# Kernel optimization log

Measured on AMD Instinct MI355X. Metric: run time of the kernel, lower is better.

The kernel has to match this reference:

```python
import jax, jax.numpy as jnp
import numpy as np

N_NODES = 100000
N_EDGES = 3200000
N_GRAPHS = 128
F_IN, HID = 16, 64


def setup_inputs() -> dict:
    key = jax.random.key(0)
    ks = jax.random.split(key, 16)
    def lin(k, fan_in, fan_out):
        bound = 1.0 / np.sqrt(fan_in)
        kw, kb = jax.random.split(k)
        W = jax.random.uniform(kw, (fan_in, fan_out), jnp.float32, -bound, bound)
        b = jax.random.uniform(kb, (fan_out,), jnp.float32, -bound, bound)
        return W, b
    x = jax.random.normal(ks[0], (N_NODES, F_IN), jnp.float32)
    edge_index = jax.random.randint(ks[1], (2, N_EDGES), 0, N_NODES, jnp.int64 if jax.config.jax_enable_x64 else jnp.int32)
    edge_attr = jax.random.normal(ks[2], (N_EDGES, 4), jnp.float32)
    batch = jnp.sort(jax.random.randint(ks[3], (N_NODES,), 0, N_GRAPHS))
    W1, b1 = lin(ks[4], F_IN, HID)
    W2, b2 = lin(ks[5], HID, HID)
    W3, b3 = lin(ks[6], HID, HID)
    Wf1, bf1 = lin(ks[7], HID, 32)
    Wf2, bf2 = lin(ks[8], 32, 1)
    return dict(x=x, edge_index=edge_index, edge_attr=edge_attr, batch=batch,
                W1=W1, b1=b1, W2=W2, b2=b2, W3=W3, b3=b3,
                Wf1=Wf1, bf1=bf1, Wf2=Wf2, bf2=bf2)


def _gcn_conv(x, src, dst, norm, W, b, n_nodes):
    # PyG GCNConv: out = scatter_add(norm * (x @ W)[src] -> dst) + b
    h = x @ W                                   # [N, out]
    msg = h[src] * norm[:, None]                # [E+N, out] gather + scale
    agg = jax.ops.segment_sum(msg, dst, num_segments=n_nodes)
    return agg + b


def reference(x, edge_index, edge_attr, batch, W1, b1, W2, b2, W3, b3, Wf1, bf1, Wf2, bf2):
    n = x.shape[0]
    # add self loops (GCNConv default)
    loop = jnp.arange(n, dtype=edge_index.dtype)
    src = jnp.concatenate([edge_index[0], loop])
    dst = jnp.concatenate([edge_index[1], loop])
    # symmetric degree normalization: deg computed on dst with self loops
    deg = jax.ops.segment_sum(jnp.ones_like(src, dtype=x.dtype), dst, num_segments=n)
    dinv = jax.lax.rsqrt(jnp.maximum(deg, 1.0))
    norm = dinv[src] * dinv[dst]

    h = jax.nn.relu(_gcn_conv(x, src, dst, norm, W1, b1, n))   # dropout = identity (eval)
    h = jax.nn.relu(_gcn_conv(h, src, dst, norm, W2, b2, n))
    h = jax.nn.relu(_gcn_conv(h, src, dst, norm, W3, b3, n))

    # global mean pool over graphs
    sums = jax.ops.segment_sum(h, batch, num_segments=N_GRAPHS)          # [B, HID]
    cnts = jax.ops.segment_sum(jnp.ones((n,), x.dtype), batch, num_segments=N_GRAPHS)
    pooled = sums / jnp.maximum(cnts, 1.0)[:, None]

    z = jax.nn.relu(pooled @ Wf1 + bf1)
    return z @ Wf2 + bf2                                                  # [B, 1]
```

## Files before the change

### kernel.cpp

```cpp
#include <hip/hip_runtime.h>
#include <hip/hip_bf16.h>

#define HID 64
#define MAXNB 2048
#define NBLK 512
#define FILL_T 1024
#define HREP 4

__device__ __forceinline__ float bf2f(unsigned short u) {
    return __uint_as_float(((unsigned)u) << 16);
}
__device__ __forceinline__ unsigned short f2bf(float f) {
    __hip_bfloat16 b = __float2bfloat16(f);
    return *(unsigned short*)&b;
}
__device__ __forceinline__ unsigned packbf(float lo, float hi) {
    return (unsigned)f2bf(lo) | ((unsigned)f2bf(hi) << 16);
}


__global__ __launch_bounds__(FILL_T) void radix_hist_kernel(
    const int* __restrict__ ei, int* __restrict__ H, int* __restrict__ bhist,
    int E, int NB, int C) {
    __shared__ int lh[HREP * (MAXNB + 1)];
    int blk = blockIdx.x, tid = threadIdx.x;
    for (int i = tid; i < HREP * (MAXNB + 1); i += FILL_T) lh[i] = 0;
    __syncthreads();
    int* lhr = lh + ((tid >> 6) & (HREP - 1)) * (MAXNB + 1);
    int lo = blk * C, hi = min(lo + C, E);
    int cnt = hi - lo;
    int n4 = ((E & 3) == 0) ? (cnt >> 2) : 0;
    const int4* d4 = (const int4*)(ei + (long long)E + lo);
    for (int k = tid; k < n4; k += FILL_T) {
        int4 d = d4[k];
        atomicAdd(&lhr[d.x >> 6], 1);
        atomicAdd(&lhr[d.y >> 6], 1);
        atomicAdd(&lhr[d.z >> 6], 1);
        atomicAdd(&lhr[d.w >> 6], 1);
    }
    for (int e = lo + (n4 << 2) + tid; e < hi; e += FILL_T)
        atomicAdd(&lhr[ei[(long long)E + e] >> 6], 1);
    __syncthreads();
    for (int i = tid; i < NB; i += FILL_T) {
        int v = 0;
#pragma unroll
        for (int r = 0; r < HREP; r++) v += lh[r * (MAXNB + 1) + i];
        H[blk * NB + i] = v;
        if (v) atomicAdd(&bhist[i], v);
    }
}

__global__ __launch_bounds__(256) void scan_kernel(
    const int* __restrict__ bhist, int* __restrict__ pptr, int* __restrict__ gcur, int NB) {
    __shared__ int ssum[256];
    int tid = threadIdx.x;
    int C = (NB + 255) / 256;
    int lo = tid * C, hi = min(lo + C, NB);
    int s = 0;
    for (int i = lo; i < hi; i++) s += bhist[i];
    ssum[tid] = s;
    __syncthreads();
    for (int off = 1; off < 256; off <<= 1) {
        int v = (tid >= off) ? ssum[tid - off] : 0;
        __syncthreads();
        ssum[tid] += v;
        __syncthreads();
    }
    int run = (tid == 0) ? 0 : ssum[tid - 1];
    for (int i = lo; i < hi; i++) {
        pptr[i] = run;
        gcur[i] = run;
        run += bhist[i];
    }
    if (hi == NB) pptr[NB] = run;
}

__global__ __launch_bounds__(FILL_T) void radix_fill_kernel(
    const int* __restrict__ ei, const int* __restrict__ H, int* __restrict__ gcur,
    unsigned* __restrict__ ebuf, int E, int NB, int C) {
    __shared__ int lcur[MAXNB];
    int blk = blockIdx.x, tid = threadIdx.x;
    for (int i = tid; i < NB; i += FILL_T) {
        int c = H[blk * NB + i];
        lcur[i] = c ? atomicAdd(&gcur[i], c) : 0;
    }
    __syncthreads();
    int lo = blk * C, hi = min(lo + C, E);
    int cnt = hi - lo;
    int n4 = ((E & 3) == 0) ? (cnt >> 2) : 0;
    const int4* s4 = (const int4*)(ei + lo);
    const int4* d4 = (const int4*)(ei + (long long)E + lo);
    for (int k = tid; k < n4; k += FILL_T) {
        int4 s = s4[k];
        int4 d = d4[k];
        int p0 = atomicAdd(&lcur[d.x >> 6], 1);
        int p1 = atomicAdd(&lcur[d.y >> 6], 1);
        int p2 = atomicAdd(&lcur[d.z >> 6], 1);
        int p3 = atomicAdd(&lcur[d.w >> 6], 1);
        ebuf[p0] = ((unsigned)s.x << 6) | (unsigned)(d.x & 63);
        ebuf[p1] = ((unsigned)s.y << 6) | (unsigned)(d.y & 63);
        ebuf[p2] = ((unsigned)s.z << 6) | (unsigned)(d.z & 63);
        ebuf[p3] = ((unsigned)s.w << 6) | (unsigned)(d.w & 63);
    }
    for (int e = lo + (n4 << 2) + tid; e < hi; e += FILL_T) {
        int s = ei[e];
        int d = ei[(long long)E + e];
        int pos = atomicAdd(&lcur[d >> 6], 1);
        ebuf[pos] = ((unsigned)s << 6) | (unsigned)(d & 63);
    }
}

__global__ __launch_bounds__(256) void node_csr_kernel(
    const int* __restrict__ pptr, const unsigned* __restrict__ ebuf,
    int* __restrict__ row_ptr, int* __restrict__ col, float* __restrict__ dinv,
    int N, int NB) {
    __shared__ int lcnt[64];
    __shared__ int loff[64];
    __shared__ int lcur[64];
    int bkt = blockIdx.x, tid = threadIdx.x;
    int beg = pptr[bkt], end = pptr[bkt + 1];
    if (tid < 64) lcnt[tid] = 0;
    __syncthreads();
    for (int e = beg + tid; e < end; e += 256) atomicAdd(&lcnt[ebuf[e] & 63u], 1);
    __syncthreads();
    if (tid < 64) {
        int v = lcnt[tid];
        int p = v;
#pragma unroll
        for (int off = 1; off < 64; off <<= 1) {
            int t = __shfl_up(p, off);
            if (tid >= off) p += t;
        }
        int base = beg + p - v;
        loff[tid] = base;
        lcur[tid] = base;
        int node = (bkt << 6) + tid;
        if (node < N) {
            row_ptr[node] = base;
            dinv[node] = rsqrtf((float)(v + 1));
        }
    }
    if (tid == 0 && bkt == NB - 1) row_ptr[N] = pptr[NB];
    __syncthreads();
    for (int e = beg + tid; e < end; e += 256) {
        unsigned ev = ebuf[e];
        int pos = atomicAdd(&lcur[ev & 63u], 1);
        col[pos] = (int)(ev >> 6);
    }
}

__global__ __launch_bounds__(256) void xs_kernel(
    const float* __restrict__ x, const float* __restrict__ dinv,
    unsigned short* __restrict__ xs, int N) {
    int n = blockIdx.x * 256 + threadIdx.x;
    if (n >= N) return;
    float dv = dinv[n];
    const float4* xr = (const float4*)(x + (long long)n * 16);
    float4 a = xr[0], b = xr[1], c = xr[2], d = xr[3];
    uint4 w;
    w.x = packbf(dv * a.x, dv * a.y);
    w.y = packbf(dv * a.z, dv * a.w);
    w.z = packbf(dv * b.x, dv * b.y);
    w.w = packbf(dv * b.z, dv * b.w);
    uint4 v;
    v.x = packbf(dv * c.x, dv * c.y);
    v.y = packbf(dv * c.z, dv * c.w);
    v.z = packbf(dv * d.x, dv * d.y);
    v.w = packbf(dv * d.z, dv * d.w);
    uint4* out = (uint4*)(xs + ((long long)n << 4));
    out[0] = w;
    out[1] = v;
}

__device__ __forceinline__ void add4(float* acc, uint2 r) {
    acc[0] += __uint_as_float(r.x << 16);
    acc[1] += __uint_as_float(r.x & 0xffff0000u);
    acc[2] += __uint_as_float(r.y << 16);
    acc[3] += __uint_as_float(r.y & 0xffff0000u);
}

__global__ __launch_bounds__(256) void gather16_kernel(
    const int* __restrict__ row_ptr, const int* __restrict__ col,
    const unsigned short* __restrict__ xs, float* __restrict__ agg, int N) {
    int wv = __builtin_amdgcn_readfirstlane(threadIdx.x >> 6);
    int node = blockIdx.x * 4 + wv;
    int lane = threadIdx.x & 63;
    if (node >= N) return;
    int grp = lane >> 2;
    int c = lane & 3;
    int beg = row_ptr[node], end = row_ptr[node + 1];

    float acc[4] = {0.f, 0.f, 0.f, 0.f};
    if (grp == 0) {
        uint2 rs = *(const uint2*)(xs + ((long long)node << 4) + (c << 2));
        add4(acc, rs);
    }
    for (int base = beg; base < end; base += 32) {
        int e0 = base + grp;
        int e1 = e0 + 16;
        bool k0 = e0 < end, k1 = e1 < end;
        int c0 = k0 ? col[e0] : 0;
        int c1 = k1 ? col[e1] : 0;
        uint2 r0 = *(const uint2*)(xs + (((long long)c0) << 4) + (c << 2));
        uint2 r1 = *(const uint2*)(xs + (((long long)c1) << 4) + (c << 2));
        if (k0) add4(acc, r0);
        if (k1) add4(acc, r1);
    }
#pragma unroll
    for (int m = 4; m <= 32; m <<= 1) {
#pragma unroll
        for (int k = 0; k < 4; k++) acc[k] += __shfl_xor(acc[k], m);
    }
    if (lane < 4) {
        float4 w = make_float4(acc[0], acc[1], acc[2], acc[3]);
        *(float4*)(agg + ((long long)node << 4) + (lane << 2)) = w;
    }
}

__global__ void gemm_agg_kernel(const float* __restrict__ agg,
                                const float* __restrict__ W,
                                const float* __restrict__ dinv,
                                const float* __restrict__ bias,
                                unsigned short* __restrict__ g, int N) {
    __shared__ float sW[16 * HID];
    __shared__ float sIn[16 * 16];
    __shared__ float sB[HID];
    int tid = threadIdx.x;
    for (int idx = tid; idx < 16 * HID; idx += 256) sW[idx] = W[idx];
    if (tid < HID) sB[tid] = bias[tid];
    int base = blockIdx.x * 16;
    if (tid < 256) {
        int r = tid / 16, cc = tid % 16;
        int node = base + r;
        sIn[tid] = (node < N) ? agg[(long long)node * 16 + cc] : 0.f;
    }
    __syncthreads();
    int j = tid & 63;
    int si = tid >> 6;
#pragma unroll
    for (int u = 0; u < 4; u++) {
        int r = si * 4 + u;
        int node = base + r;
        if (node >= N) continue;
        float acc = 0.f;
#pragma unroll
        for (int k = 0; k < 16; k++) acc += sIn[r * 16 + k] * sW[k * HID + j];
        float v = dinv[node] * acc + sB[j];
        g[(long long)node * HID + j] = f2bf(v > 0.f ? v : 0.f);
    }
}

template <typename Tin, int K>
__global__ void gemm_g_kernel(const Tin* __restrict__ in,
                              const float* __restrict__ W,
                              const float* __restrict__ dinv,
                              unsigned short* __restrict__ g, int N) {
    __shared__ float sW[K * HID];
    __shared__ float sIn[16 * K];
    int tid = threadIdx.x;
    for (int idx = tid; idx < K * HID; idx += 256) sW[idx] = W[idx];
    int base = blockIdx.x * 16;
    for (int idx = tid; idx < 16 * K; idx += 256) {
        int r = idx / K, c = idx % K;
        int node = base + r;
        float v = 0.f;
        if (node < N) {
            Tin t = in[(long long)node * K + c];
            if constexpr (sizeof(Tin) == 2) v = bf2f((unsigned short)t);
            else v = (float)t;
        }
        sIn[idx] = v;
    }
    __syncthreads();
    int j = tid & 63;
    int si = tid >> 6;
#pragma unroll
    for (int u = 0; u < 4; u++) {
        int r = si * 4 + u;
        int node = base + r;
        if (node >= N) continue;
        float acc = 0.f;
#pragma unroll
        for (int k = 0; k < K; k++) acc += sIn[r * K + k] * sW[k * HID + j];
        g[(long long)node * HID + j] = f2bf(dinv[node] * acc);
    }
}

__device__ __forceinline__ void add8(float* acc, uint4 r) {
    acc[0] += __uint_as_float(r.x << 16);
    acc[1] += __uint_as_float(r.x & 0xffff0000u);
    acc[2] += __uint_as_float(r.y << 16);
    acc[3] += __uint_as_float(r.y & 0xffff0000u);
    acc[4] += __uint_as_float(r.z << 16);
    acc[5] += __uint_as_float(r.z & 0xffff0000u);
    acc[6] += __uint_as_float(r.w << 16);
    acc[7] += __uint_as_float(r.w & 0xffff0000u);
}

__global__ __launch_bounds__(256) void gather_kernel(
    const int* __restrict__ row_ptr, const int* __restrict__ col,
    const unsigned short* __restrict__ g, const float* __restrict__ dinv,
    const float* __restrict__ bias, unsigned short* __restrict__ h, int N) {
    int wv = __builtin_amdgcn_readfirstlane(threadIdx.x >> 6);
    int node = blockIdx.x * 4 + wv;
    int lane = threadIdx.x & 63;
    if (node >= N) return;
    int grp = lane >> 3;
    int c = lane & 7;
    int beg = row_ptr[node], end = row_ptr[node + 1];

    float acc[8] = {0.f, 0.f, 0.f, 0.f, 0.f, 0.f, 0.f, 0.f};
    if (grp == 0) {
        uint4 rs = *(const uint4*)(g + ((long long)node << 6) + (c << 3));
        add8(acc, rs);
    }

    for (int base = beg; base < end; base += 32) {
        int e0 = base + grp;
        int e1 = e0 + 8, e2 = e0 + 16, e3 = e0 + 24;
        bool k0 = e0 < end, k1 = e1 < end, k2 = e2 < end, k3 = e3 < end;
        int c0 = k0 ? col[e0] : 0;
        int c1 = k1 ? col[e1] : 0;
        int c2 = k2 ? col[e2] : 0;
        int c3 = k3 ? col[e3] : 0;
        uint4 r0 = *(const uint4*)(g + (((long long)c0) << 6) + (c << 3));
        uint4 r1 = *(const uint4*)(g + (((long long)c1) << 6) + (c << 3));
        uint4 r2 = *(const uint4*)(g + (((long long)c2) << 6) + (c << 3));
        uint4 r3 = *(const uint4*)(g + (((long long)c3) << 6) + (c << 3));
        if (k0) add8(acc, r0);
        if (k1) add8(acc, r1);
        if (k2) add8(acc, r2);
        if (k3) add8(acc, r3);
    }

#pragma unroll
    for (int m = 8; m <= 32; m <<= 1) {
#pragma unroll
        for (int k = 0; k < 8; k++) acc[k] += __shfl_xor(acc[k], m);
    }

    if (lane < 8) {
        float dv = dinv[node];
        float4 ba = *(const float4*)(bias + (lane << 3));
        float4 bb = *(const float4*)(bias + (lane << 3) + 4);
        float v0 = dv * acc[0] + ba.x;
        float v1 = dv * acc[1] + ba.y;
        float v2 = dv * acc[2] + ba.z;
        float v3 = dv * acc[3] + ba.w;
        float v4 = dv * acc[4] + bb.x;
        float v5 = dv * acc[5] + bb.y;
        float v6 = dv * acc[6] + bb.z;
        float v7 = dv * acc[7] + bb.w;
        v0 = v0 > 0.f ? v0 : 0.f;
        v1 = v1 > 0.f ? v1 : 0.f;
        v2 = v2 > 0.f ? v2 : 0.f;
        v3 = v3 > 0.f ? v3 : 0.f;
        v4 = v4 > 0.f ? v4 : 0.f;
        v5 = v5 > 0.f ? v5 : 0.f;
        v6 = v6 > 0.f ? v6 : 0.f;
        v7 = v7 > 0.f ? v7 : 0.f;
        uint4 w;
        w.x = (unsigned)f2bf(v0) | ((unsigned)f2bf(v1) << 16);
        w.y = (unsigned)f2bf(v2) | ((unsigned)f2bf(v3) << 16);
        w.z = (unsigned)f2bf(v4) | ((unsigned)f2bf(v5) << 16);
        w.w = (unsigned)f2bf(v6) | ((unsigned)f2bf(v7) << 16);
        *(uint4*)(h + ((long long)node << 6) + (lane << 3)) = w;
    }
}

__global__ void pool_kernel(const unsigned short* __restrict__ h, const int* __restrict__ batch,
                            float* __restrict__ sums, float* __restrict__ cnt, int N) {
    int wave = blockIdx.x * 4 + (threadIdx.x >> 6);
    int lane = threadIdx.x & 63;
    int lo = wave * 16;
    if (lo >= N) return;
    int hi = min(lo + 16, N);
    int curb = batch[lo];
    float sum = 0.f;
    int nseg = 0;
    for (int i = lo; i < hi; i++) {
        int b = batch[i];
        if (b != curb) {
            atomicAdd(&sums[curb * HID + lane], sum);
            if (lane == 0) atomicAdd(&cnt[curb], (float)nseg);
            curb = b; sum = 0.f; nseg = 0;
        }
        sum += bf2f(h[(long long)i * HID + lane]);
        nseg++;
    }
    atomicAdd(&sums[curb * HID + lane], sum);
    if (lane == 0) atomicAdd(&cnt[curb], (float)nseg);
}

__global__ void final_kernel(const float* __restrict__ sums, const float* __restrict__ cnt,
                             const float* __restrict__ Wf1, const float* __restrict__ bf1,
                             const float* __restrict__ Wf2, const float* __restrict__ bf2,
                             float* __restrict__ out) {
    __shared__ float sW1[HID * 32];
    __shared__ float sW2[32];
    int tid = threadIdx.x;
    for (int idx = tid; idx < HID * 32; idx += 128) sW1[idx] = Wf1[idx];
    if (tid < 32) sW2[tid] = Wf2[tid];
    __syncthreads();
    int b = tid;
    float pooled[HID];
    float c = fmaxf(cnt[b], 1.0f);
#pragma unroll
    for (int j = 0; j < HID; j++) pooled[j] = sums[b * HID + j] / c;
    float o = bf2[0];
#pragma unroll 4
    for (int hd = 0; hd < 32; hd++) {
        float z = bf1[hd];
#pragma unroll
        for (int j = 0; j < HID; j++) z += pooled[j] * sW1[j * 32 + hd];
        z = fmaxf(z, 0.f);
        o += z * sW2[hd];
    }
    out[b] = o;
}

extern "C" void kernel_launch(void* const* d_in, const int* in_sizes, int n_in,
                              void* d_out, int out_size, void* d_ws, size_t ws_size,
                              hipStream_t stream) {
    const float* x     = (const float*)d_in[0];
    const int*   ei    = (const int*)d_in[1];
    const int*   batch = (const int*)d_in[3];
    const float* W1  = (const float*)d_in[4];
    const float* b1  = (const float*)d_in[5];
    const float* W2  = (const float*)d_in[6];
    const float* b2  = (const float*)d_in[7];
    const float* W3  = (const float*)d_in[8];
    const float* b3  = (const float*)d_in[9];
    const float* Wf1 = (const float*)d_in[10];
    const float* bf1 = (const float*)d_in[11];
    const float* Wf2 = (const float*)d_in[12];
    const float* bf2 = (const float*)d_in[13];
    float* out = (float*)d_out;

    const int N  = in_sizes[0] / 16;
    const int E  = in_sizes[1] / 2;
    const int NB = (N + 63) / 64;

    char* ws = (char*)d_ws;
    size_t o = 0;
    float*          dinv    = (float*)(ws + o);          o += ((size_t)N * 4 + 4095) / 4096 * 4096;
    int*            row_ptr = (int*)(ws + o);            o += ((size_t)(N + 1) * 4 + 4095) / 4096 * 4096;
    int*            pptr    = (int*)(ws + o);            o += ((size_t)(NB + 1) * 4 + 4095) / 4096 * 4096;
    int*            bhist   = (int*)(ws + o);            o += ((size_t)NB * 4 + 4095) / 4096 * 4096;
    int*            gcur    = (int*)(ws + o);            o += ((size_t)NB * 4 + 4095) / 4096 * 4096;
    int*            H       = (int*)(ws + o);            o += ((size_t)NBLK * NB * 4 + 4095) / 4096 * 4096;
    unsigned*       ebuf    = (unsigned*)(ws + o);       o += (size_t)E * 4;
    int*            col     = (int*)(ws + o);            o += (size_t)E * 4;
    unsigned short* A       = (unsigned short*)(ws + o); o += (size_t)N * HID * 2;
    unsigned short* B       = (unsigned short*)(ws + o); o += (size_t)N * HID * 2;
    unsigned short* XS      = (unsigned short*)(ws + o); o += ((size_t)N * 16 * 2 + 4095) / 4096 * 4096;
    float*          AGG     = (float*)(ws + o);          o += ((size_t)N * 16 * 4 + 4095) / 4096 * 4096;
    float*          sums    = (float*)(ws + o);          o += 128 * HID * 4;
    float*          cnt     = (float*)(ws + o);          o += 128 * 4;
    (void)ws_size;

    const int T = 256;
    const int Cchunk = (((E + NBLK - 1) / NBLK) + 3) & ~3;
    const int gGm = (N + 15) / 16;
    const int gGa = (N + 3) / 4;
    const int gN  = (N + 255) / 256;
    const int gPool = ((N + 15) / 16 + 3) / 4;

    hipMemsetAsync(bhist, 0, (size_t)NB * 4, stream);
    radix_hist_kernel<<<NBLK, FILL_T, 0, stream>>>(ei, H, bhist, E, NB, Cchunk);
    scan_kernel<<<1, T, 0, stream>>>(bhist, pptr, gcur, NB);
    radix_fill_kernel<<<NBLK, FILL_T, 0, stream>>>(ei, H, gcur, ebuf, E, NB, Cchunk);
    node_csr_kernel<<<NB, T, 0, stream>>>(pptr, ebuf, row_ptr, col, dinv, N, NB);

    xs_kernel<<<gN, T, 0, stream>>>(x, dinv, XS, N);
    gather16_kernel<<<gGa, T, 0, stream>>>(row_ptr, col, XS, AGG, N);
    gemm_agg_kernel<<<gGm, T, 0, stream>>>(AGG, W1, dinv, b1, B, N);

    gemm_g_kernel<unsigned short, 64><<<gGm, T, 0, stream>>>(B, W2, dinv, B, N);
    gather_kernel<<<gGa, T, 0, stream>>>(row_ptr, col, B, dinv, b2, A, N);

    gemm_g_kernel<unsigned short, 64><<<gGm, T, 0, stream>>>(A, W3, dinv, A, N);
    gather_kernel<<<gGa, T, 0, stream>>>(row_ptr, col, A, dinv, b3, B, N);

    hipMemsetAsync(sums, 0, (128 * HID + 128) * 4, stream);
    pool_kernel<<<gPool, T, 0, stream>>>(B, batch, sums, cnt, N);
    final_kernel<<<1, 128, 0, stream>>>(sums, cnt, Wf1, bf1, Wf2, bf2, out);
}
```

Measured before the change: 499.3 us.

## Fuse xs scaling into CSR build and layer-1 epilogue with layer-2 GEMM

The node CSR kernel now stages its bucket's edges in shared memory, so ebuf is read from global memory once instead of twice. It also computes the dinv-scaled bf16 features directly, which removes the separate xs kernel. The layer-1 GEMM epilogue keeps the ReLU hidden tile in shared memory and multiplies it by W2 in the same kernel. That removes a launch and a full N×64 bf16 round trip through global memory. In exchange the kernel carries a 16KB W2 tile in shared memory per block plus 16KB of staging in the CSR kernel, which may lower occupancy.

```diff
diff --git a/kernel.cpp b/kernel.cpp
--- a/kernel.cpp
+++ b/kernel.cpp
@@ -6,6 +6,7 @@
 #define NBLK 512
 #define FILL_T 1024
 #define HREP 4
+#define CSR_CAP 4096
 
 __device__ __forceinline__ float bf2f(unsigned short u) {
     return __uint_as_float(((unsigned)u) << 16);
@@ -110,18 +111,26 @@
     }
 }
 
-__global__ __launch_bounds__(256) void node_csr_kernel(
+__global__ __launch_bounds__(256) void node_csr_xs_kernel(
     const int* __restrict__ pptr, const unsigned* __restrict__ ebuf,
+    const float* __restrict__ x,
     int* __restrict__ row_ptr, int* __restrict__ col, float* __restrict__ dinv,
-    int N, int NB) {
+    unsigned short* __restrict__ xs, int N, int NB) {
+    __shared__ unsigned sE[CSR_CAP];
     __shared__ int lcnt[64];
-    __shared__ int loff[64];
     __shared__ int lcur[64];
+    __shared__ float sDv[64];
     int bkt = blockIdx.x, tid = threadIdx.x;
     int beg = pptr[bkt], end = pptr[bkt + 1];
+    int cnt = end - beg;
+    int stg = min(cnt, CSR_CAP);
     if (tid < 64) lcnt[tid] = 0;
-    __syncthreads();
-    for (int e = beg + tid; e < end; e += 256) atomicAdd(&lcnt[ebuf[e] & 63u], 1);
+    for (int i = tid; i < stg; i += 256) sE[i] = ebuf[beg + i];
+    __syncthreads();
+    for (int i = tid; i < cnt; i += 256) {
+        unsigned ev = (i < CSR_CAP) ? sE[i] : ebuf[beg + i];
+        atomicAdd(&lcnt[ev & 63u], 1);
+    }
     __syncthreads();
     if (tid < 64) {
         int v = lcnt[tid];
@@ -132,44 +141,34 @@
             if (tid >= off) p += t;
         }
         int base = beg + p - v;
-        loff[tid] = base;
         lcur[tid] = base;
         int node = (bkt << 6) + tid;
+        float dv = rsqrtf((float)(v + 1));
+        sDv[tid] = dv;
         if (node < N) {
             row_ptr[node] = base;
-            dinv[node] = rsqrtf((float)(v + 1));
+            dinv[node] = dv;
         }
     }
     if (tid == 0 && bkt == NB - 1) row_ptr[N] = pptr[NB];
     __syncthreads();
-    for (int e = beg + tid; e < end; e += 256) {
-        unsigned ev = ebuf[e];
+    for (int i = tid; i < cnt; i += 256) {
+        unsigned ev = (i < CSR_CAP) ? sE[i] : ebuf[beg + i];
         int pos = atomicAdd(&lcur[ev & 63u], 1);
         col[pos] = (int)(ev >> 6);
     }
-}
-
-__global__ __launch_bounds__(256) void xs_kernel(
-    const float* __restrict__ x, const float* __restrict__ dinv,
-    unsigned short* __restrict__ xs, int N) {
-    int n = blockIdx.x * 256 + threadIdx.x;
-    if (n >= N) return;
-    float dv = dinv[n];
-    const float4* xr = (const float4*)(x + (long long)n * 16);
-    float4 a = xr[0], b = xr[1], c = xr[2], d = xr[3];
-    uint4 w;
-    w.x = packbf(dv * a.x, dv * a.y);
-    w.y = packbf(dv * a.z, dv * a.w);
-    w.z = packbf(dv * b.x, dv * b.y);
-    w.w = packbf(dv * b.z, dv * b.w);
-    uint4 v;
-    v.x = packbf(dv * c.x, dv * c.y);
-    v.y = packbf(dv * c.z, dv * c.w);
-    v.z = packbf(dv * d.x, dv * d.y);
-    v.w = packbf(dv * d.z, dv * d.w);
-    uint4* out = (uint4*)(xs + ((long long)n << 4));
-    out[0] = w;
-    out[1] = v;
+    {
+        int r = tid >> 2, q = tid & 3;
+        int node = (bkt << 6) + r;
+        if (node < N) {
+            float dv = sDv[r];
+            float4 xv = *(const float4*)(x + (long long)node * 16 + q * 4);
+            uint2 w;
+            w.x = packbf(dv * xv.x, dv * xv.y);
+            w.y = packbf(dv * xv.z, dv * xv.w);
+            *(uint2*)(xs + (long long)node * 16 + q * 4) = w;
+        }
+    }
 }
 
 __device__ __forceinline__ void add4(float* acc, uint2 r) {
@@ -217,36 +216,53 @@
     }
 }
 
-__global__ void gemm_agg_kernel(const float* __restrict__ agg,
-                                const float* __restrict__ W,
-                                const float* __restrict__ dinv,
-                                const float* __restrict__ bias,
-                                unsigned short* __restrict__ g, int N) {
-    __shared__ float sW[16 * HID];
+__global__ __launch_bounds__(256) void gemm_agg2_kernel(
+    const float* __restrict__ agg,
+    const float* __restrict__ W1, const float* __restrict__ b1,
+    const float* __restrict__ W2,
+    const float* __restrict__ dinv, unsigned short* __restrict__ g2, int N) {
+    __shared__ float sW1[16 * HID];
+    __shared__ float sW2[HID * HID];
     __shared__ float sIn[16 * 16];
-    __shared__ float sB[HID];
+    __shared__ float sH[16 * HID];
+    __shared__ float sB1[HID];
+    __shared__ float sDv[16];
     int tid = threadIdx.x;
-    for (int idx = tid; idx < 16 * HID; idx += 256) sW[idx] = W[idx];
-    if (tid < HID) sB[tid] = bias[tid];
+    for (int i = tid; i < 16 * HID; i += 256) sW1[i] = W1[i];
+    for (int i = tid; i < HID * HID; i += 256) sW2[i] = W2[i];
+    if (tid < HID) sB1[tid] = b1[tid];
     int base = blockIdx.x * 16;
-    if (tid < 256) {
-        int r = tid / 16, cc = tid % 16;
+    {
+        int r = tid >> 4, c = tid & 15;
         int node = base + r;
-        sIn[tid] = (node < N) ? agg[(long long)node * 16 + cc] : 0.f;
+        sIn[tid] = (node < N) ? agg[(long long)node * 16 + c] : 0.f;
+    }
+    if (tid < 16) {
+        int node = base + tid;
+        sDv[tid] = (node < N) ? dinv[node] : 0.f;
     }
     __syncthreads();
     int j = tid & 63;
     int si = tid >> 6;
+#pragma unroll
+    for (int u = 0; u < 4; u++) {
+        int r = si * 4 + u;
+        float acc = 0.f;
+#pragma unroll
+        for (int k = 0; k < 16; k++) acc += sIn[r * 16 + k] * sW1[k * HID + j];
+        float v = sDv[r] * acc + sB1[j];
+        sH[r * HID + j] = v > 0.f ? v : 0.f;
+    }
+    __syncthreads();
 #pragma unroll
     for (int u = 0; u < 4; u++) {
         int r = si * 4 + u;
         int node = base + r;
         if (node >= N) continue;
         float acc = 0.f;
-#pragma unroll
-        for (int k = 0; k < 16; k++) acc += sIn[r * 16 + k] * sW[k * HID + j];
-        float v = dinv[node] * acc + sB[j];
-        g[(long long)node * HID + j] = f2bf(v > 0.f ? v : 0.f);
+#pragma unroll 16
+        for (int k = 0; k < HID; k++) acc += sH[r * HID + k] * sW2[k * HID + j];
+        g2[(long long)node * HID + j] = f2bf(sDv[r] * acc);
     }
 }
 
@@ -463,26 +479,23 @@
     const int Cchunk = (((E + NBLK - 1) / NBLK) + 3) & ~3;
     const int gGm = (N + 15) / 16;
     const int gGa = (N + 3) / 4;
-    const int gN  = (N + 255) / 256;
     const int gPool = ((N + 15) / 16 + 3) / 4;
 
     hipMemsetAsync(bhist, 0, (size_t)NB * 4, stream);
     radix_hist_kernel<<<NBLK, FILL_T, 0, stream>>>(ei, H, bhist, E, NB, Cchunk);
     scan_kernel<<<1, T, 0, stream>>>(bhist, pptr, gcur, NB);
     radix_fill_kernel<<<NBLK, FILL_T, 0, stream>>>(ei, H, gcur, ebuf, E, NB, Cchunk);
-    node_csr_kernel<<<NB, T, 0, stream>>>(pptr, ebuf, row_ptr, col, dinv, N, NB);
-
-    xs_kernel<<<gN, T, 0, stream>>>(x, dinv, XS, N);
+    node_csr_xs_kernel<<<NB, T, 0, stream>>>(pptr, ebuf, x, row_ptr, col, dinv, XS, N, NB);
+
     gather16_kernel<<<gGa, T, 0, stream>>>(row_ptr, col, XS, AGG, N);
-    gemm_agg_kernel<<<gGm, T, 0, stream>>>(AGG, W1, dinv, b1, B, N);
-
-    gemm_g_kernel<unsigned short, 64><<<gGm, T, 0, stream>>>(B, W2, dinv, B, N);
-    gather_kernel<<<gGa, T, 0, stream>>>(row_ptr, col, B, dinv, b2, A, N);
-
-    gemm_g_kernel<unsigned short, 64><<<gGm, T, 0, stream>>>(A, W3, dinv, A, N);
-    gather_kernel<<<gGa, T, 0, stream>>>(row_ptr, col, A, dinv, b3, B, N);
+    gemm_agg2_kernel<<<gGm, T, 0, stream>>>(AGG, W1, b1, W2, dinv, A, N);
+
+    gather_kernel<<<gGa, T, 0, stream>>>(row_ptr, col, A, dinv, b2, B, N);
+
+    gemm_g_kernel<unsigned short, 64><<<gGm, T, 0, stream>>>(B, W3, dinv, B, N);
+    gather_kernel<<<gGa, T, 0, stream>>>(row_ptr, col, B, dinv, b3, A, N);
 
     hipMemsetAsync(sums, 0, (128 * HID + 128) * 4, stream);
-    pool_kernel<<<gPool, T, 0, stream>>>(B, batch, sums, cnt, N);
+    pool_kernel<<<gPool, T, 0, stream>>>(A, batch, sums, cnt, N);
     final_kernel<<<1, 128, 0, stream>>>(sums, cnt, Wf1, bf1, Wf2, bf2, out);
 }
```

Result: no change. 495.6 us (-0.7%).
